# Performance work log

Measured on AMD Instinct MI355X. Metric: run time of the kernel, lower is better.

The kernel has to match this reference:

```python
import jax, jax.numpy as jnp
import numpy as np

MARGIN = 0.2
MEM = 1000  # memory_size
EPS = 1e-12  # F.normalize eps


def _nearest_ds(x, h, w):
    # torch F.interpolate(mode='nearest'): src_idx = floor(dst_idx * H / h)
    B, H, W = x.shape
    ri = (jnp.arange(h) * H) // h
    ci = (jnp.arange(w) * W) // w
    return x[:, ri][:, :, ci]


def _first_k(mask, k):
    # Deterministic stand-in for randperm sampling: keep the first k True entries.
    rank = jnp.cumsum(mask.astype(jnp.int32)) - 1
    return mask & (rank < k), rank


def setup_inputs() -> dict:
    key = jax.random.key(0)
    k = jax.random.split(key, 6)
    B, C, H, W = 8, 21, 512, 512
    D, h, w = 128, 128, 128
    return {
        "preds": jax.random.normal(k[0], (B, C, H, W), jnp.float32),
        "embeddings": jax.random.normal(k[1], (B, D, h, w), jnp.float32),
        "gts": jax.random.randint(k[2], (B, H, W), 0, 21, dtype=jnp.int32),
        "fsss_gts": jax.random.randint(k[3], (B, H, W), 0, 256, dtype=jnp.int32),
        "pos_memory": jax.random.normal(k[4], (MEM, D), jnp.float32),
        "neg_memory": jax.random.normal(k[5], (MEM, D), jnp.float32),
    }


def reference(preds, embeddings, gts, fsss_gts, pos_memory, neg_memory):
    B, D, h, w = embeddings.shape
    M = pos_memory.shape[0]

    # downsample label maps / predicted classes to the feature resolution (nearest)
    s_pred = _nearest_ds(jnp.argmax(preds, axis=1).astype(jnp.float32), h, w).reshape(-1)
    s_fsss = _nearest_ds(fsss_gts.astype(jnp.float32), h, w).reshape(-1)
    # s_gt is computed in the original but unused for the loss.

    # L2-normalize embeddings over channel dim, flatten to [N, D] (channel-last)
    norm = jnp.sqrt(jnp.sum(embeddings * embeddings, axis=1, keepdims=True))
    emb = embeddings / jnp.maximum(norm, EPS)
    E = emb.transpose(1, 0, 2, 3).reshape(D, -1).T  # [N, D], N = B*h*w

    pred_mask = s_pred != 0
    fsss_mask = (s_fsss != 0) & (s_fsss != 255)
    ignore_mask = s_fsss == 255
    anchor_mask = pred_mask & fsss_mask
    positive_mask = fsss_mask ^ anchor_mask
    negative_mask = pred_mask ^ ((fsss_mask | ignore_mask) & pred_mask)

    sel_anc, _ = _first_k(anchor_mask, M // 10)
    sel_pos, rank_pos = _first_k(positive_mask, M // 3)
    sel_neg, rank_neg = _first_k(negative_mask, M // 3)

    # circular-buffer update (ptr=0): scatter selected (detached) embeddings into slots rank%M
    Ed = jax.lax.stop_gradient(E)
    idx_pos = jnp.where(sel_pos, rank_pos % M, M)  # M -> dropped
    idx_neg = jnp.where(sel_neg, rank_neg % M, M)
    pos_mem = pos_memory.at[idx_pos].set(Ed, mode='drop')
    neg_mem = neg_memory.at[idx_neg].set(Ed, mode='drop')

    # mean over all (anchor, memory) similarity pairs factorizes:
    # mean_{a,m} a.m = (sum_a a) . (sum_m m) / (Na * M)
    anc_sum = jnp.einsum('nd,n->d', E, sel_anc.astype(E.dtype))
    n_anc = jnp.maximum(jnp.sum(sel_anc.astype(E.dtype)), 1.0)
    pos_mean = jnp.dot(anc_sum, jnp.sum(pos_mem, axis=0)) / (n_anc * M)
    neg_mean = jnp.dot(anc_sum, jnp.sum(neg_mem, axis=0)) / (n_anc * M)

    return jax.nn.relu(pos_mean - neg_mean + MARGIN)
```

## Files before the change

kernel.cpp:

```cpp
#include <hip/hip_runtime.h>
#include <stdint.h>


#define NPOS  131072
#define NBLK  512
#define MEMSZ 1000
#define KANC  100
#define KPN   333
#define SLOT_POS 100
#define SLOT_NEG 433
#define FIX_SCALE 1099511627776.0
#define INV_FIX   (1.0 / 1099511627776.0)

#define OFF_FLAGS   0
#define OFF_COUNTS  131072
#define OFF_IDX     137216
#define OFF_TOTALS  140288
#define OFF_ACCUM   140304
#define OFF_CTR     152592

__global__ __launch_bounds__(256) void mask_kernel(
    const float* __restrict__ preds,
    const int* __restrict__ fsss,
    uint8_t* __restrict__ flags,
    int* __restrict__ blockCounts,
    unsigned long long* __restrict__ accum,
    unsigned int* __restrict__ counterB)
{
    const int tid = threadIdx.x, blk = blockIdx.x;
    const int lane = tid & 63, wave = tid >> 6;
    const int n = blk * 256 + tid;
    const int b = n >> 14;
    const int ij = n & 16383;
    const int row = (ij >> 7) << 2;
    const int col = (ij & 127) << 2;

    const float* p = preds + (size_t)b * 21 * 262144 + (size_t)row * 512 + col;
    float best = __builtin_nontemporal_load(p);
    int bc = 0;
#pragma unroll
    for (int c = 1; c < 21; ++c) {
        float v = __builtin_nontemporal_load(p + (size_t)c * 262144);
        if (v > best) { best = v; bc = c; }
    }
    const int fv = __builtin_nontemporal_load(
        fsss + (size_t)b * 262144 + (size_t)row * 512 + col);

    const bool pm = (bc != 0);
    const bool fm = (fv != 0) && (fv != 255);
    const int myflag = (int)(pm && fm)
                     | ((int)(!pm && fm) << 1)
                     | ((int)(pm && (fv == 0)) << 2);
    flags[n] = (uint8_t)myflag;

    __shared__ int s_i[12];
#pragma unroll
    for (int cat = 0; cat < 3; ++cat) {
        unsigned long long m = __ballot((myflag >> cat) & 1);
        if (lane == 0) s_i[cat * 4 + wave] = (int)__popcll(m);
    }
    __syncthreads();
    if (tid < 3)
        blockCounts[tid * NBLK + blk] =
            s_i[tid * 4] + s_i[tid * 4 + 1] + s_i[tid * 4 + 2] + s_i[tid * 4 + 3];

    if (blk == 0) {
        for (int i = tid; i < 4 * 3 * 128; i += 256) accum[i] = 0ull;
        if (tid == 0) *counterB = 0u;
    }
}

__global__ __launch_bounds__(256) void select_kernel(
    const uint8_t* __restrict__ flags,
    const int* __restrict__ blockCounts,
    int* __restrict__ idx,
    int* __restrict__ totals)
{
    const int tid = threadIdx.x, blk = blockIdx.x;
    const int lane = tid & 63, wave = tid >> 6;
    __shared__ int s_i[12];

#pragma unroll
    for (int cat = 0; cat < 3; ++cat) {
        const int c0 = blockCounts[cat * NBLK + tid];
        const int c1 = blockCounts[cat * NBLK + 256 + tid];
        int v = ((tid < blk) ? c0 : 0) + ((256 + tid < blk) ? c1 : 0);
#pragma unroll
        for (int off = 1; off < 64; off <<= 1) v += __shfl_xor(v, off, 64);
        if (lane == 0) s_i[cat * 4 + wave] = v;
    }
    __syncthreads();
    int pre[3];
#pragma unroll
    for (int cat = 0; cat < 3; ++cat)
        pre[cat] = s_i[cat * 4] + s_i[cat * 4 + 1] + s_i[cat * 4 + 2] + s_i[cat * 4 + 3];
    if (blk == NBLK - 1 && tid < 3)
        totals[tid] = pre[tid] + blockCounts[tid * NBLK + NBLK - 1];
    __syncthreads();

    const int n = blk * 256 + tid;
    const int f = flags[n];
    unsigned long long masks[3];
#pragma unroll
    for (int cat = 0; cat < 3; ++cat) {
        masks[cat] = __ballot((f >> cat) & 1);
        if (lane == 0) s_i[cat * 4 + wave] = (int)__popcll(masks[cat]);
    }
    __syncthreads();
    const int kcap[3]  = {KANC, KPN, KPN};
    const int basec[3] = {0, SLOT_POS, SLOT_NEG};
#pragma unroll
    for (int cat = 0; cat < 3; ++cat) {
        if ((f >> cat) & 1) {
            int woff = 0;
#pragma unroll
            for (int w = 0; w < 4; ++w) if (w < wave) woff += s_i[cat * 4 + w];
            const int intra = woff + (int)__popcll(masks[cat] & ((1ull << lane) - 1ull));
            const int rank = pre[cat] + intra;
            if (rank < kcap[cat]) idx[basec[cat] + rank] = n;
        }
    }
}

__global__ __launch_bounds__(256) void gather_final_kernel(
    const float* __restrict__ emb,
    const float* __restrict__ posMem,
    const float* __restrict__ negMem,
    const int* __restrict__ idx,
    const int* __restrict__ totals,
    unsigned long long* __restrict__ accum,
    unsigned int* __restrict__ counterB,
    float* __restrict__ out)
{
    const int tid = threadIdx.x, blk = blockIdx.x;
    const int lane = tid & 63, wave = tid >> 6;
    const int d = tid & 127;
    const int A = min(KANC, totals[0]);
    const int P = min(KPN, totals[1]);
    const int Q = min(KPN, totals[2]);

    if (blk < 383) {
        const int half = tid >> 7;
        const int slot = blk * 2 + half;
        int cat; bool valid;
        if (slot < SLOT_POS)      { cat = 0; valid = slot < A; }
        else if (slot < SLOT_NEG) { cat = 1; valid = (slot - SLOT_POS) < P; }
        else                      { cat = 2; valid = (slot - SLOT_NEG) < Q; }

        float v = 0.f;
        if (valid) {
            const int nn = idx[slot];
            v = emb[((size_t)(nn >> 14) * 128 + d) * 16384 + (nn & 16383)];
        }
        float sq = v * v;
#pragma unroll
        for (int off = 1; off < 64; off <<= 1) sq += __shfl_xor(sq, off, 64);
        __shared__ float s_f[4];
        if (lane == 0) s_f[wave] = sq;
        __syncthreads();
        const float nrm2 = s_f[half * 2] + s_f[half * 2 + 1];
        if (valid) {
            const float scale = 1.0f / fmaxf(sqrtf(nrm2), 1e-12f);
            const long long fx =
                (long long)llrint((double)v * (double)scale * FIX_SCALE);
            atomicAdd(&accum[(((blk & 3) * 3 + cat) << 7) + d],
                      (unsigned long long)fx);
        }
    } else {
        const int t = blk - 383;
        const int memSel = t >> 3;
        const int part = t & 7;
        const float* mem = memSel ? negMem : posMem;
        const int cnt = memSel ? Q : P;
        const int rowHalf = tid >> 7;
        const int m0 = part * 125;
        double acc = 0.0;
        for (int r = rowHalf; r < 125; r += 2) {
            const int m = m0 + r;
            if (m >= cnt) acc += (double)mem[(size_t)m * 128 + d];
        }
        const long long fx = (long long)llrint(acc * FIX_SCALE);
        atomicAdd(&accum[(((blk & 3) * 3 + (memSel ? 2 : 1)) << 7) + d],
                  (unsigned long long)fx);
    }

    __threadfence();
    __syncthreads();
    __shared__ int s_fin;
    if (tid == 0) {
        unsigned old = atomicAdd(counterB, 1u);
        s_fin = (old == 398) ? 1 : 0;
    }
    __syncthreads();
    if (!s_fin) return;
    __threadfence();

    __shared__ double s_d[2];
    if (tid < 128) {
        double anc = 0.0, pos = 0.0, neg = 0.0;
#pragma unroll
        for (int s = 0; s < 4; ++s) {
            anc += (double)(long long)accum[((s * 3 + 0) << 7) + tid];
            pos += (double)(long long)accum[((s * 3 + 1) << 7) + tid];
            neg += (double)(long long)accum[((s * 3 + 2) << 7) + tid];
        }
        double prod = anc * (pos - neg) * (INV_FIX * INV_FIX);
#pragma unroll
        for (int off = 1; off < 64; off <<= 1) prod += __shfl_xor(prod, off, 64);
        if (lane == 0) s_d[wave] = prod;
    }
    __syncthreads();
    if (tid == 0) {
        const double red = s_d[0] + s_d[1];
        const double nAnc = (A > 0) ? (double)A : 1.0;
        const double vv = red / (nAnc * (double)MEMSZ) + 0.2;
        out[0] = (float)(vv > 0.0 ? vv : 0.0);
    }
}

extern "C" void kernel_launch(void* const* d_in, const int* in_sizes, int n_in,
                              void* d_out, int out_size, void* d_ws, size_t ws_size,
                              hipStream_t stream) {
    const float* preds  = (const float*)d_in[0];
    const float* emb    = (const float*)d_in[1];
    const int* fsss     = (const int*)d_in[3];
    const float* posMem = (const float*)d_in[4];
    const float* negMem = (const float*)d_in[5];
    float* out = (float*)d_out;

    char* ws = (char*)d_ws;
    uint8_t* flags      = (uint8_t*)(ws + OFF_FLAGS);
    int* blockCounts    = (int*)(ws + OFF_COUNTS);
    int* idx            = (int*)(ws + OFF_IDX);
    int* totals         = (int*)(ws + OFF_TOTALS);
    unsigned long long* accum = (unsigned long long*)(ws + OFF_ACCUM);
    unsigned int* ctr   = (unsigned int*)(ws + OFF_CTR);

    mask_kernel  <<<NBLK, 256, 0, stream>>>(preds, fsss, flags, blockCounts,
                                            accum, ctr);
    select_kernel<<<NBLK, 256, 0, stream>>>(flags, blockCounts, idx, totals);
    gather_final_kernel<<<399, 256, 0, stream>>>(emb, posMem, negMem, idx, totals,
                                                 accum, ctr, out);
}
```

Before: 50.37 us.

## Fuse selection into gather kernel via per-block prefix scan and binary search

Removes the separate select kernel. Each gather block now recomputes the exclusive prefix sums of per-block category counts in shared memory, binary-searches for the source block of its slot's rank, and re-ballots that block's flags to find the exact pixel index. This saves one kernel launch and the global idx/totals round trip. In exchange, every one of the 399 blocks redundantly scans 1536 counts and does extra synchronisation and flag reads.

Result: faster. 49.11 us (-2.5%).

```diff
diff --git a/kernel.cpp b/kernel.cpp
--- a/kernel.cpp
+++ b/kernel.cpp
@@ -14,10 +14,8 @@
 
 #define OFF_FLAGS   0
 #define OFF_COUNTS  131072
-#define OFF_IDX     137216
-#define OFF_TOTALS  140288
-#define OFF_ACCUM   140304
-#define OFF_CTR     152592
+#define OFF_ACCUM   137216
+#define OFF_CTR     149504
 
 __global__ __launch_bounds__(256) void mask_kernel(
     const float* __restrict__ preds,
@@ -70,88 +68,91 @@
     }
 }
 
-__global__ __launch_bounds__(256) void select_kernel(
-    const uint8_t* __restrict__ flags,
-    const int* __restrict__ blockCounts,
-    int* __restrict__ idx,
-    int* __restrict__ totals)
-{
-    const int tid = threadIdx.x, blk = blockIdx.x;
-    const int lane = tid & 63, wave = tid >> 6;
-    __shared__ int s_i[12];
-
-#pragma unroll
-    for (int cat = 0; cat < 3; ++cat) {
-        const int c0 = blockCounts[cat * NBLK + tid];
-        const int c1 = blockCounts[cat * NBLK + 256 + tid];
-        int v = ((tid < blk) ? c0 : 0) + ((256 + tid < blk) ? c1 : 0);
-#pragma unroll
-        for (int off = 1; off < 64; off <<= 1) v += __shfl_xor(v, off, 64);
-        if (lane == 0) s_i[cat * 4 + wave] = v;
-    }
-    __syncthreads();
-    int pre[3];
-#pragma unroll
-    for (int cat = 0; cat < 3; ++cat)
-        pre[cat] = s_i[cat * 4] + s_i[cat * 4 + 1] + s_i[cat * 4 + 2] + s_i[cat * 4 + 3];
-    if (blk == NBLK - 1 && tid < 3)
-        totals[tid] = pre[tid] + blockCounts[tid * NBLK + NBLK - 1];
-    __syncthreads();
-
-    const int n = blk * 256 + tid;
-    const int f = flags[n];
-    unsigned long long masks[3];
-#pragma unroll
-    for (int cat = 0; cat < 3; ++cat) {
-        masks[cat] = __ballot((f >> cat) & 1);
-        if (lane == 0) s_i[cat * 4 + wave] = (int)__popcll(masks[cat]);
-    }
-    __syncthreads();
-    const int kcap[3]  = {KANC, KPN, KPN};
-    const int basec[3] = {0, SLOT_POS, SLOT_NEG};
-#pragma unroll
-    for (int cat = 0; cat < 3; ++cat) {
-        if ((f >> cat) & 1) {
-            int woff = 0;
-#pragma unroll
-            for (int w = 0; w < 4; ++w) if (w < wave) woff += s_i[cat * 4 + w];
-            const int intra = woff + (int)__popcll(masks[cat] & ((1ull << lane) - 1ull));
-            const int rank = pre[cat] + intra;
-            if (rank < kcap[cat]) idx[basec[cat] + rank] = n;
-        }
-    }
-}
-
-__global__ __launch_bounds__(256) void gather_final_kernel(
+__global__ __launch_bounds__(256) void select_gather_final_kernel(
     const float* __restrict__ emb,
     const float* __restrict__ posMem,
     const float* __restrict__ negMem,
-    const int* __restrict__ idx,
-    const int* __restrict__ totals,
+    const uint8_t* __restrict__ flags,
+    const int* __restrict__ blockCounts,
     unsigned long long* __restrict__ accum,
     unsigned int* __restrict__ counterB,
     float* __restrict__ out)
 {
     const int tid = threadIdx.x, blk = blockIdx.x;
     const int lane = tid & 63, wave = tid >> 6;
+
+    __shared__ int s_pre[3 * NBLK];
+    __shared__ int s_tot[3];
+    __shared__ int s_w[4];
+#pragma unroll 1
+    for (int cat = 0; cat < 3; ++cat) {
+        const int c0 = blockCounts[cat * NBLK + 2 * tid];
+        const int c1 = blockCounts[cat * NBLK + 2 * tid + 1];
+        const int pairsum = c0 + c1;
+        int incl = pairsum;
+#pragma unroll
+        for (int off = 1; off < 64; off <<= 1) {
+            int v = __shfl_up(incl, off, 64);
+            if (lane >= off) incl += v;
+        }
+        if (lane == 63) s_w[wave] = incl;
+        __syncthreads();
+        int woff = 0;
+#pragma unroll
+        for (int w = 0; w < 4; ++w) if (w < wave) woff += s_w[w];
+        const int excl0 = woff + incl - pairsum;
+        s_pre[cat * NBLK + 2 * tid]     = excl0;
+        s_pre[cat * NBLK + 2 * tid + 1] = excl0 + c0;
+        if (tid == 0) s_tot[cat] = s_w[0] + s_w[1] + s_w[2] + s_w[3];
+        __syncthreads();
+    }
+    const int A = min(KANC, s_tot[0]);
+    const int P = min(KPN, s_tot[1]);
+    const int Q = min(KPN, s_tot[2]);
     const int d = tid & 127;
-    const int A = min(KANC, totals[0]);
-    const int P = min(KPN, totals[1]);
-    const int Q = min(KPN, totals[2]);
 
     if (blk < 383) {
+        __shared__ int s_nn[2];
+        int nnv[2];
+#pragma unroll 1
+        for (int h = 0; h < 2; ++h) {
+            const int slot = blk * 2 + h;
+            int cat, r;
+            if (slot < SLOT_POS)      { cat = 0; r = slot; }
+            else if (slot < SLOT_NEG) { cat = 1; r = slot - SLOT_POS; }
+            else                      { cat = 2; r = slot - SLOT_NEG; }
+            const int cnt = (cat == 0) ? A : ((cat == 1) ? P : Q);
+            if (r < cnt) {
+                int lo = 0, hi = NBLK - 1;
+                while (lo < hi) {
+                    const int mid = (lo + hi + 1) >> 1;
+                    if (s_pre[cat * NBLK + mid] <= r) lo = mid; else hi = mid - 1;
+                }
+                const int bb = lo;
+                const int lr = r - s_pre[cat * NBLK + bb];
+                const int bit = (flags[bb * 256 + tid] >> cat) & 1;
+                const unsigned long long m = __ballot(bit);
+                if (lane == 0) s_w[wave] = (int)__popcll(m);
+                __syncthreads();
+                int woff = 0;
+#pragma unroll
+                for (int w = 0; w < 4; ++w) if (w < wave) woff += s_w[w];
+                const int intra = woff + (int)__popcll(m & ((1ull << lane) - 1ull));
+                if (bit && intra == lr) s_nn[h] = bb * 256 + tid;
+                __syncthreads();
+                nnv[h] = s_nn[h];
+            } else {
+                nnv[h] = -1;
+            }
+        }
+
         const int half = tid >> 7;
         const int slot = blk * 2 + half;
-        int cat; bool valid;
-        if (slot < SLOT_POS)      { cat = 0; valid = slot < A; }
-        else if (slot < SLOT_NEG) { cat = 1; valid = (slot - SLOT_POS) < P; }
-        else                      { cat = 2; valid = (slot - SLOT_NEG) < Q; }
-
+        const int cat = (slot < SLOT_POS) ? 0 : ((slot < SLOT_NEG) ? 1 : 2);
+        const int nn = nnv[half];
         float v = 0.f;
-        if (valid) {
-            const int nn = idx[slot];
+        if (nn >= 0)
             v = emb[((size_t)(nn >> 14) * 128 + d) * 16384 + (nn & 16383)];
-        }
         float sq = v * v;
 #pragma unroll
         for (int off = 1; off < 64; off <<= 1) sq += __shfl_xor(sq, off, 64);
@@ -159,7 +160,7 @@
         if (lane == 0) s_f[wave] = sq;
         __syncthreads();
         const float nrm2 = s_f[half * 2] + s_f[half * 2 + 1];
-        if (valid) {
+        if (nn >= 0) {
             const float scale = 1.0f / fmaxf(sqrtf(nrm2), 1e-12f);
             const long long fx =
                 (long long)llrint((double)v * (double)scale * FIX_SCALE);
@@ -231,14 +232,12 @@
     char* ws = (char*)d_ws;
     uint8_t* flags      = (uint8_t*)(ws + OFF_FLAGS);
     int* blockCounts    = (int*)(ws + OFF_COUNTS);
-    int* idx            = (int*)(ws + OFF_IDX);
-    int* totals         = (int*)(ws + OFF_TOTALS);
     unsigned long long* accum = (unsigned long long*)(ws + OFF_ACCUM);
     unsigned int* ctr   = (unsigned int*)(ws + OFF_CTR);
 
-    mask_kernel  <<<NBLK, 256, 0, stream>>>(preds, fsss, flags, blockCounts,
-                                            accum, ctr);
-    select_kernel<<<NBLK, 256, 0, stream>>>(flags, blockCounts, idx, totals);
-    gather_final_kernel<<<399, 256, 0, stream>>>(emb, posMem, negMem, idx, totals,
-                                                 accum, ctr, out);
+    mask_kernel<<<NBLK, 256, 0, stream>>>(preds, fsss, flags, blockCounts,
+                                          accum, ctr);
+    select_gather_final_kernel<<<399, 256, 0, stream>>>(emb, posMem, negMem,
+                                                        flags, blockCounts,
+                                                        accum, ctr, out);
 }
```
